# Kernel tuning notes

Hardware: AMD Instinct MI355X
Metric: run time of the kernel (lower is better)

The kernel has to match this reference:

```python
import jax, jax.numpy as jnp
import numpy as np

B, T, NI, NH, NO = 32, 2048, 1, 512, 1


def setup_inputs() -> dict:
    key = jax.random.key(0)
    ks = jax.random.split(key, 7)
    x = jax.random.normal(ks[0], (B, T, NI), dtype=jnp.float32)
    # torch code draws h_0 ~ U[-1,1) once and tiles over batch; here per-batch uniform
    h_0 = jax.random.uniform(ks[1], (B, NH), dtype=jnp.float32) * 2.0 - 1.0
    w_input_std = 1.0 / np.sqrt(NH)
    W_ih = jax.random.normal(ks[2], (NH, NI), dtype=jnp.float32) * w_input_std
    prob_c = 0.1
    w_hidden_std = 1.5 / np.sqrt(prob_c * NH)
    mask = jax.random.bernoulli(ks[3], prob_c, (NH, NH)).astype(jnp.float32)
    W_hh = jax.random.normal(ks[4], (NH, NH), dtype=jnp.float32) * w_hidden_std * mask
    W_hz = jax.random.normal(ks[5], (NO, NH), dtype=jnp.float32) * w_input_std
    W_zh = jax.random.uniform(ks[6], (NH, NO), dtype=jnp.float32, minval=-1.0, maxval=1.0)
    return {"x": x, "h_0": h_0, "W_ih": W_ih, "W_hh": W_hh, "W_hz": W_hz, "W_zh": W_zh}


def reference(x, h_0, W_ih, W_hh, W_hz, W_zh):
    dt, tau = 0.001, 0.01
    alpha = dt / tau  # 0.1
    # precompute input projection for all timesteps: [T, B, NH]
    x_proj = jnp.einsum('bti,hi->tbh', x, W_ih)

    def step(carry, xp_t):
        h_prev, z_prev = carry  # [B,NH], [B,NO]
        h_transfer = jnp.tanh(h_prev)
        dhdt = -h_prev + h_transfer @ W_hh.T + xp_t + z_prev @ W_zh.T
        h_t = h_prev + alpha * dhdt
        z_t = jnp.tanh(h_t) @ W_hz.T
        return (h_t, z_t), (h_t, z_t)

    z0 = jnp.tanh(h_0) @ W_hz.T
    _, (h, z) = jax.lax.scan(step, (h_0, z0), x_proj)
    # scan stacks time first -> [T,B,*]; transpose to [B,T,*]
    return jnp.swapaxes(z, 0, 1), jnp.swapaxes(h, 0, 1)
```

## Files before the change

### kernel.cpp

```cpp
#include <hip/hip_runtime.h>


#define NH   512
#define TT   2048
#define BB   32
#define PAD  96
#define PIN  80

__global__ __launch_bounds__(512) void count_nnz(
    const float* __restrict__ Whh, int* __restrict__ nnz) {
  const int wib  = threadIdx.x >> 6;
  const int lane = threadIdx.x & 63;
  const int row  = blockIdx.x * 8 + wib;
  const float* wrow = Whh + (size_t)row * NH;
  int cnt = 0;
  for (int c = 0; c < NH / 64; ++c)
    cnt += __popcll(__ballot(wrow[c * 64 + lane] != 0.0f));
  if (lane == 0) nnz[row] = cnt;
}

__global__ __launch_bounds__(512) void sort_rows(
    const int* __restrict__ nnz, int* __restrict__ perm) {
  __shared__ int nl[NH];
  const int j = threadIdx.x;
  const int my = nnz[j];
  nl[j] = my;
  __syncthreads();
  int r = 0;
  const int4* p4 = (const int4*)nl;
  for (int i = 0; i < NH / 4; ++i) {
    int4 v = p4[i];
    const int base = i * 4;
    r += (v.x > my) || (v.x == my && base + 0 < j);
    r += (v.y > my) || (v.y == my && base + 1 < j);
    r += (v.z > my) || (v.z == my && base + 2 < j);
    r += (v.w > my) || (v.w == my && base + 3 < j);
  }
  perm[r] = j;
}

__global__ __launch_bounds__(64) void build_schedule(
    const float* __restrict__ Whh, const int* __restrict__ perm,
    float* __restrict__ vals, unsigned* __restrict__ offs,
    int* __restrict__ cntw) {
  __shared__ int claim[2][32];
  const int lane = threadIdx.x;
  const int wid  = blockIdx.x;
  const int p    = wid * 64 + lane;
  const int half = lane >> 5;
  const int home = lane & 31;
  const int row  = perm[p];
  const float* wrow = Whh + (size_t)row * NH;

  unsigned occ32[16];
  int remaining = 0;
  unsigned nonempty = 0;
  #pragma unroll
  for (int r = 0; r < 16; ++r) {
    unsigned lo = 0, hi = 0;
    #pragma unroll
    for (int m = 0; m < 16; ++m) {
      lo |= (wrow[(2 * r)     + 32 * m] != 0.f) ? (1u << m) : 0u;
      hi |= (wrow[(2 * r + 1) + 32 * m] != 0.f) ? (1u << m) : 0u;
    }
    occ32[r] = lo | (hi << 16);
    remaining += __popc(lo) + __popc(hi);
    if (lo) nonempty |= 1u << (2 * r);
    if (hi) nonempty |= 1u << (2 * r + 1);
  }

  int s = 0;
  while (__ballot(remaining > 0) != 0ull && s < PAD) {
    claim[half][home] = 0;
    __builtin_amdgcn_wave_barrier();

    bool placed = false;
    int  mybank = 0;
    unsigned excl = 0;
    const int key = (remaining << 8) | (lane + 1);

    for (int round = 0; round < 12; ++round) {
      unsigned cand = (placed || remaining == 0) ? 0u : (nonempty & ~excl);
      bool want = cand != 0u;
      int bl = 0;
      if (want) {
        unsigned rot = home ? ((cand >> home) | (cand << (32 - home))) : cand;
        bl = (home + __ffs(rot) - 1) & 31;
      }
      if (__ballot(want) == 0ull) break;
      if (want) atomicMax(&claim[half][bl], key);
      __builtin_amdgcn_wave_barrier();
      if (want) {
        int c = ((volatile int*)claim[half])[bl];
        if (c == key) {
          placed = true; mybank = bl;
          ((volatile int*)claim[half])[bl] = 0x7FFFFFFF;
        } else {
          excl |= 1u << bl;
        }
      }
      __builtin_amdgcn_wave_barrier();
    }

    if (!placed && remaining > 0 && (PAD - s) <= remaining) {
      placed = true;
      mybank = __ffs(nonempty) - 1;
    }

    float v = 0.f; unsigned col = 0u;
    if (placed) {
      #pragma unroll
      for (int r = 0; r < 16; ++r) {
        if (r == (mybank >> 1)) {
          unsigned w   = occ32[r];
          unsigned m16 = (mybank & 1) ? (w >> 16) : (w & 0xFFFFu);
          int m = __ffs(m16) - 1;
          col = (unsigned)(mybank + 32 * m);
          unsigned nm = m16 & (m16 - 1u);
          occ32[r] = (mybank & 1) ? ((w & 0x0000FFFFu) | (nm << 16))
                                  : ((w & 0xFFFF0000u) | nm);
          if (nm == 0u) nonempty &= ~(1u << mybank);
        }
      }
      v = wrow[col];
      --remaining;
    }
    vals[s * NH + p] = v;
    offs[s * NH + p] = col;
    ++s;
  }
  if (lane == 0) cntw[wid] = s;
  for (int e = s; e < PAD; ++e) {
    vals[e * NH + p] = 0.f;
    offs[e * NH + p] = 0u;
  }
}

template <int CTRL, int RM>
__device__ __forceinline__ float dppadd(float v) {
  int t = __builtin_amdgcn_update_dpp(0, __float_as_int(v), CTRL, RM, 0xF, true);
  return v + __int_as_float(t);
}
__device__ __forceinline__ float wave_sum_lane63(float v) {
  v = dppadd<0xB1,  0xF>(v);
  v = dppadd<0x4E,  0xF>(v);
  v = dppadd<0x141, 0xF>(v);
  v = dppadd<0x140, 0xF>(v);
  v = dppadd<0x142, 0xA>(v);
  v = dppadd<0x143, 0xC>(v);
  return v;
}

__device__ __forceinline__ float ftanh(float x) {
  float xc = fminf(9.0f, fmaxf(-9.0f, x));
  float t  = __expf(2.0f * xc);
  return (t - 1.0f) * __builtin_amdgcn_rcpf(t + 1.0f);
}

#define GA(T_RD, E) (*(const float*)((const char*)(T_RD) + cidx[E]))

#define ESN_STEP(T_RD, T_WR, RWR, SIDX)                                      \
  {                                                                          \
    float d0 = 0.f, d1 = 0.f, d2 = 0.f, d3 = 0.f;                            \
    _Pragma("unroll")                                                        \
    for (int e = 0; e < PAD; e += 8) {                                       \
      if (e < cw) {                                                          \
        d0 = fmaf(wval[e + 0], GA(T_RD, e + 0), d0);                         \
        d1 = fmaf(wval[e + 1], GA(T_RD, e + 1), d1);                         \
        d2 = fmaf(wval[e + 2], GA(T_RD, e + 2), d2);                         \
        d3 = fmaf(wval[e + 3], GA(T_RD, e + 3), d3);                         \
        d0 = fmaf(wval[e + 4], GA(T_RD, e + 4), d0);                         \
        d1 = fmaf(wval[e + 5], GA(T_RD, e + 5), d1);                         \
        d2 = fmaf(wval[e + 6], GA(T_RD, e + 6), d2);                         \
        d3 = fmaf(wval[e + 7], GA(T_RD, e + 7), d3);                         \
      }                                                                      \
    }                                                                        \
    float dot  = (d0 + d1) + (d2 + d3);                                      \
    float xp   = x_lds[SIDX] * w_ih;                                         \
    float dhdt = ((dot - h) + xp) + z_prev * w_zh;                           \
    float hn   = h + 0.1f * dhdt;                                            \
    float thn  = ftanh(hn);                                                  \
    T_WR[row] = thn;                                                         \
    oh[(SIDX) * NH + row] = hn;                                              \
    float pzs = wave_sum_lane63(thn * w_hz);                                 \
    if (lane == 63) red[RWR][wid] = pzs;                                     \
    asm volatile("s_waitcnt lgkmcnt(0)\n\ts_barrier" ::: "memory");          \
    float4 r0 = *(const float4*)&red[RWR][0];                                \
    float4 r1 = *(const float4*)&red[RWR][4];                                \
    float z = ((r0.x + r0.y) + (r0.z + r0.w)) + ((r1.x + r1.y) + (r1.z + r1.w)); \
    if (p == 0) oz[SIDX] = z;                                                \
    z_prev = z; h = hn;                                                      \
  }

__global__ __launch_bounds__(512, 2) void esn_steps(
    const float* __restrict__ x,   const float* __restrict__ h0,
    const float* __restrict__ Wih, const float* __restrict__ Whz,
    const float* __restrict__ Wzh, const float* __restrict__ vals,
    const unsigned* __restrict__ offs, const int* __restrict__ perm,
    const int* __restrict__ cntw, float* __restrict__ out) {
  __shared__ float t_lds[2][NH];
  __shared__ float x_lds[TT];
  __shared__ __align__(16) float red[2][8];

  const int p    = threadIdx.x;
  const int b    = blockIdx.x;
  const int lane = p & 63;
  const int wid  = p >> 6;
  const int row  = perm[p];

  float* t0 = t_lds[0];
  float* t1 = t_lds[1];

  for (int i = p; i < TT; i += NH) x_lds[i] = x[(size_t)b * TT + i];

  int cw = __builtin_amdgcn_readfirstlane((cntw[wid] + 7) & ~7);

  float    wval[PAD];
  unsigned cidx[PAD];
  #pragma unroll
  for (int e = 0; e < PAD; ++e) {
    wval[e] = vals[e * NH + p];
    cidx[e] = offs[e * NH + p] * 4u;
  }
  #pragma unroll
  for (int e = 0; e < PIN; ++e)
    asm volatile("" : "+v"(wval[e]), "+v"(cidx[e]));

  const float w_ih = Wih[row];
  const float w_hz = Whz[row];
  const float w_zh = Wzh[row];
  float h = h0[(size_t)b * NH + row];

  float* oz = out + (size_t)b * TT;
  float* oh = out + (size_t)BB * TT + (size_t)b * TT * NH;

  float th0 = ftanh(h);
  t0[row] = th0;
  float pz = wave_sum_lane63(th0 * w_hz);
  if (lane == 63) red[0][wid] = pz;
  __syncthreads();
  float4 i0 = *(const float4*)&red[0][0];
  float4 i1 = *(const float4*)&red[0][4];
  float z_prev = ((i0.x + i0.y) + (i0.z + i0.w)) + ((i1.x + i1.y) + (i1.z + i1.w));

  for (int s = 0; s < TT; s += 2) {
    ESN_STEP(t0, t1, 1, s);
    ESN_STEP(t1, t0, 0, s + 1);
  }
}

extern "C" void kernel_launch(void* const* d_in, const int* in_sizes, int n_in,
                              void* d_out, int out_size, void* d_ws,
                              size_t ws_size, hipStream_t stream) {
  const float* x   = (const float*)d_in[0];
  const float* h0  = (const float*)d_in[1];
  const float* Wih = (const float*)d_in[2];
  const float* Whh = (const float*)d_in[3];
  const float* Whz = (const float*)d_in[4];
  const float* Wzh = (const float*)d_in[5];
  float* out = (float*)d_out;

  float*    vals = (float*)d_ws;
  unsigned* offs = (unsigned*)(vals + PAD * NH);
  int*      nnz  = (int*)(offs + PAD * NH);
  int*      perm = nnz + NH;
  int*      cntw = perm + NH;

  hipLaunchKernelGGL(count_nnz, dim3(NH / 8), dim3(512), 0, stream, Whh, nnz);
  hipLaunchKernelGGL(sort_rows, dim3(1), dim3(512), 0, stream, nnz, perm);
  hipLaunchKernelGGL(build_schedule, dim3(8), dim3(64), 0, stream,
                     Whh, perm, vals, offs, cntw);
  hipLaunchKernelGGL(esn_steps, dim3(BB), dim3(512), 0, stream,
                     x, h0, Wih, Whz, Wzh, vals, offs, perm, cntw, out);
}
```

Before: 2.640 ms.

## Replace greedy bank-claim scheduler with bipartite edge coloring for sparse W_hh

The per-slot greedy bank-claiming scheduler is replaced by a bipartite edge-coloring routine that uses alternating-path recoloring (in the style of König's theorem) to assign each nonzero of a row to a slot. No two lanes in a half-wave then read the same LDS bank in the same slot. The goal is to shrink the number of padded slots (cntw) and remove bank conflicts in the recurrent sparse matvec that runs for every timestep. The cost is a serial single-thread coloring in the setup kernel, which adds preprocessing latency on every call.

Result: slower. 3.196 ms (+21.0%).

```diff
diff --git a/kernel.cpp b/kernel.cpp
--- a/kernel.cpp
+++ b/kernel.cpp
@@ -6,6 +6,7 @@
 #define BB   32
 #define PAD  96
 #define PIN  80
+#define NONE_ 0xFF
 
 __global__ __launch_bounds__(512) void count_nnz(
     const float* __restrict__ Whh, int* __restrict__ nnz) {
@@ -39,100 +40,158 @@
   perm[r] = j;
 }
 
-__global__ __launch_bounds__(64) void build_schedule(
+__global__ __launch_bounds__(64) void build_color(
     const float* __restrict__ Whh, const int* __restrict__ perm,
     float* __restrict__ vals, unsigned* __restrict__ offs,
     int* __restrict__ cntw) {
-  __shared__ int claim[2][32];
+  __shared__ unsigned short occ[64][32];
+  __shared__ unsigned char  mL[2][32][PAD];
+  __shared__ unsigned char  mB[2][32][PAD];
+  __shared__ unsigned freeL[2][32][3];
+  __shared__ unsigned freeB[2][32][3];
+  __shared__ short pB[2][128], pL[2][128];
+  __shared__ int cwsh;
+
   const int lane = threadIdx.x;
-  const int wid  = blockIdx.x;
-  const int p    = wid * 64 + lane;
-  const int half = lane >> 5;
-  const int home = lane & 31;
+  const int g    = blockIdx.x;
+  const int p    = g * 64 + lane;
+  const int hl   = lane >> 5;
+  const int li   = lane & 31;
   const int row  = perm[p];
   const float* wrow = Whh + (size_t)row * NH;
 
-  unsigned occ32[16];
-  int remaining = 0;
-  unsigned nonempty = 0;
+  if (lane == 0) cwsh = 0;
+  for (int b = 0; b < 32; ++b) {
+    unsigned m16 = 0;
+    for (int m = 0; m < 16; ++m)
+      m16 |= (wrow[b + 32 * m] != 0.f) ? (1u << m) : 0u;
+    occ[lane][b] = (unsigned short)m16;
+  }
+  for (int c = 0; c < PAD; ++c) { mL[hl][li][c] = NONE_; mB[hl][li][c] = NONE_; }
   #pragma unroll
-  for (int r = 0; r < 16; ++r) {
-    unsigned lo = 0, hi = 0;
-    #pragma unroll
-    for (int m = 0; m < 16; ++m) {
-      lo |= (wrow[(2 * r)     + 32 * m] != 0.f) ? (1u << m) : 0u;
-      hi |= (wrow[(2 * r + 1) + 32 * m] != 0.f) ? (1u << m) : 0u;
-    }
-    occ32[r] = lo | (hi << 16);
-    remaining += __popc(lo) + __popc(hi);
-    if (lo) nonempty |= 1u << (2 * r);
-    if (hi) nonempty |= 1u << (2 * r + 1);
-  }
-
-  int s = 0;
-  while (__ballot(remaining > 0) != 0ull && s < PAD) {
-    claim[half][home] = 0;
-    __builtin_amdgcn_wave_barrier();
-
-    bool placed = false;
-    int  mybank = 0;
-    unsigned excl = 0;
-    const int key = (remaining << 8) | (lane + 1);
-
-    for (int round = 0; round < 12; ++round) {
-      unsigned cand = (placed || remaining == 0) ? 0u : (nonempty & ~excl);
-      bool want = cand != 0u;
-      int bl = 0;
-      if (want) {
-        unsigned rot = home ? ((cand >> home) | (cand << (32 - home))) : cand;
-        bl = (home + __ffs(rot) - 1) & 31;
-      }
-      if (__ballot(want) == 0ull) break;
-      if (want) atomicMax(&claim[half][bl], key);
-      __builtin_amdgcn_wave_barrier();
-      if (want) {
-        int c = ((volatile int*)claim[half])[bl];
-        if (c == key) {
-          placed = true; mybank = bl;
-          ((volatile int*)claim[half])[bl] = 0x7FFFFFFF;
-        } else {
-          excl |= 1u << bl;
+  for (int w2 = 0; w2 < 3; ++w2) {
+    freeL[hl][li][w2] = 0xFFFFFFFFu;
+    freeB[hl][li][w2] = 0xFFFFFFFFu;
+  }
+  __syncthreads();
+
+  if (li == 0) {
+    int maxc = 0;
+    for (int l = 0; l < 32; ++l) {
+      const int gl = hl * 32 + l;
+      for (int b = 0; b < 32; ++b) {
+        const int mult = __popc((unsigned)occ[gl][b]);
+        for (int m = 0; m < mult; ++m) {
+          int c = -1;
+          #pragma unroll
+          for (int w2 = 0; w2 < 3; ++w2) {
+            unsigned cm = freeL[hl][l][w2] & freeB[hl][b][w2];
+            if (cm) { c = w2 * 32 + __ffs(cm) - 1; break; }
+          }
+          if (c >= 0) {
+            mL[hl][l][c] = (unsigned char)b;
+            mB[hl][b][c] = (unsigned char)l;
+            freeL[hl][l][c >> 5] &= ~(1u << (c & 31));
+            freeB[hl][b][c >> 5] &= ~(1u << (c & 31));
+            if (c > maxc) maxc = c;
+            continue;
+          }
+          int a = -1, be = -1;
+          #pragma unroll
+          for (int w2 = 0; w2 < 3; ++w2) {
+            unsigned mm = freeL[hl][l][w2];
+            if (mm) { a = w2 * 32 + __ffs(mm) - 1; break; }
+          }
+          #pragma unroll
+          for (int w2 = 0; w2 < 3; ++w2) {
+            unsigned mm = freeB[hl][b][w2];
+            if (mm) { be = w2 * 32 + __ffs(mm) - 1; break; }
+          }
+          if (a < 0) continue;
+          if (be < 0) {
+            mL[hl][l][a] = (unsigned char)b;
+            freeL[hl][l][a >> 5] &= ~(1u << (a & 31));
+            if (a > maxc) maxc = a;
+            continue;
+          }
+          int n = 0, curN = b, curCol = a, isbank = 1, of = 0;
+          for (;;) {
+            int nxt = isbank ? (int)mB[hl][curN][curCol]
+                             : (int)mL[hl][curN][curCol];
+            if (nxt == NONE_) break;
+            if (n >= 128) { of = 1; break; }
+            pB[hl][n] = (short)(isbank ? curN : nxt);
+            pL[hl][n] = (short)(isbank ? nxt : curN);
+            ++n;
+            curN = nxt; isbank ^= 1;
+            curCol = (curCol == a) ? be : a;
+          }
+          if (of) {
+            mL[hl][l][a] = (unsigned char)b;
+            freeL[hl][l][a >> 5] &= ~(1u << (a & 31));
+            if (a > maxc) maxc = a;
+            continue;
+          }
+          for (int i = 0; i < n; ++i) {
+            int oc = (i & 1) ? be : a;
+            mB[hl][pB[hl][i]][oc] = NONE_;
+            mL[hl][pL[hl][i]][oc] = NONE_;
+          }
+          for (int i = 0; i < n; ++i) {
+            int nc = (i & 1) ? a : be;
+            mB[hl][pB[hl][i]][nc] = (unsigned char)pL[hl][i];
+            mL[hl][pL[hl][i]][nc] = (unsigned char)pB[hl][i];
+          }
+          freeB[hl][b][a >> 5]  ^= (1u << (a & 31));
+          freeB[hl][b][be >> 5] ^= (1u << (be & 31));
+          if (isbank) {
+            freeB[hl][curN][a >> 5]  ^= (1u << (a & 31));
+            freeB[hl][curN][be >> 5] ^= (1u << (be & 31));
+          } else {
+            freeL[hl][curN][a >> 5]  ^= (1u << (a & 31));
+            freeL[hl][curN][be >> 5] ^= (1u << (be & 31));
+          }
+          mL[hl][l][a] = (unsigned char)b;
+          mB[hl][b][a] = (unsigned char)l;
+          freeL[hl][l][a >> 5] &= ~(1u << (a & 31));
+          freeB[hl][b][a >> 5] &= ~(1u << (a & 31));
+          if (a > maxc) maxc = a;
         }
       }
-      __builtin_amdgcn_wave_barrier();
     }
-
-    if (!placed && remaining > 0 && (PAD - s) <= remaining) {
-      placed = true;
-      mybank = __ffs(nonempty) - 1;
+    atomicMax(&cwsh, maxc + 1);
+  }
+  __syncthreads();
+
+  for (int b = 0; b < 32; ++b) {
+    int need = __popc((unsigned)occ[lane][b]);
+    int have = 0;
+    for (int c = 0; c < PAD; ++c) have += (mL[hl][li][c] == b);
+    while (have < need) {
+      for (int c = 0; c < PAD; ++c)
+        if (mL[hl][li][c] == NONE_) {
+          mL[hl][li][c] = (unsigned char)b;
+          atomicMax(&cwsh, c + 1);
+          break;
+        }
+      ++have;
     }
-
+  }
+  __syncthreads();
+  if (lane == 0) cntw[g] = cwsh;
+
+  for (int c = 0; c < PAD; ++c) {
+    int b = mL[hl][li][c];
     float v = 0.f; unsigned col = 0u;
-    if (placed) {
-      #pragma unroll
-      for (int r = 0; r < 16; ++r) {
-        if (r == (mybank >> 1)) {
-          unsigned w   = occ32[r];
-          unsigned m16 = (mybank & 1) ? (w >> 16) : (w & 0xFFFFu);
-          int m = __ffs(m16) - 1;
-          col = (unsigned)(mybank + 32 * m);
-          unsigned nm = m16 & (m16 - 1u);
-          occ32[r] = (mybank & 1) ? ((w & 0x0000FFFFu) | (nm << 16))
-                                  : ((w & 0xFFFF0000u) | nm);
-          if (nm == 0u) nonempty &= ~(1u << mybank);
-        }
-      }
+    if (b != NONE_) {
+      unsigned m16 = (unsigned)occ[lane][b];
+      int m = __ffs(m16) - 1;
+      occ[lane][b] = (unsigned short)(m16 & (m16 - 1u));
+      col = (unsigned)(b + 32 * m);
       v = wrow[col];
-      --remaining;
     }
-    vals[s * NH + p] = v;
-    offs[s * NH + p] = col;
-    ++s;
-  }
-  if (lane == 0) cntw[wid] = s;
-  for (int e = s; e < PAD; ++e) {
-    vals[e * NH + p] = 0.f;
-    offs[e * NH + p] = 0u;
+    vals[c * NH + p] = v;
+    offs[c * NH + p] = col;
   }
 }
 
@@ -268,7 +327,7 @@
 
   hipLaunchKernelGGL(count_nnz, dim3(NH / 8), dim3(512), 0, stream, Whh, nnz);
   hipLaunchKernelGGL(sort_rows, dim3(1), dim3(512), 0, stream, nnz, perm);
-  hipLaunchKernelGGL(build_schedule, dim3(8), dim3(64), 0, stream,
+  hipLaunchKernelGGL(build_color, dim3(8), dim3(64), 0, stream,
                      Whh, perm, vals, offs, cntw);
   hipLaunchKernelGGL(esn_steps, dim3(BB), dim3(512), 0, stream,
                      x, h0, Wih, Whz, Wzh, vals, offs, perm, cntw, out);
```

## Balance bank load across wave halves and prefer dense banks in sparse schedule

Applied to the files above, without the earlier changes.

The sparse W_hh schedule builder now runs as one 512-thread block. Within each wave it greedily reorders rows so that the two 32-lane halves carry balanced per-bank loads, which produces a second permutation used by the step kernel. The per-slot bank claim now prefers banks that still hold many nonzeros (at least 4, then at least 2) and runs fewer claim rounds. The goal is fewer padded slots per wave (a lower cntw) and fewer LDS bank conflicts in the recurrent gather, at the cost of a slower single-block preprocessing kernel.

Measured after the change: 2.679 ms. Within noise of the previous version (+1.5%).

```diff
diff --git a/kernel.cpp b/kernel.cpp
--- a/kernel.cpp
+++ b/kernel.cpp
@@ -39,98 +39,148 @@
   perm[r] = j;
 }
 
-__global__ __launch_bounds__(64) void build_schedule(
+__global__ __launch_bounds__(512) void build_psched(
     const float* __restrict__ Whh, const int* __restrict__ perm,
-    float* __restrict__ vals, unsigned* __restrict__ offs,
-    int* __restrict__ cntw) {
-  __shared__ int claim[2][32];
-  const int lane = threadIdx.x;
-  const int wid  = blockIdx.x;
-  const int p    = wid * 64 + lane;
-  const int half = lane >> 5;
-  const int home = lane & 31;
-  const int row  = perm[p];
+    int* __restrict__ perm2, float* __restrict__ vals,
+    unsigned* __restrict__ offs, int* __restrict__ cntw) {
+  __shared__ unsigned short occ[8][64][32];
+  __shared__ unsigned char  lorder[8][64];
+  __shared__ int   claim[8][2][32];
+  __shared__ short bload[8][2][32];
+  __shared__ short cnth[8][2];
+
+  const int tid  = threadIdx.x;
+  const int w    = tid >> 6;
+  const int lane = tid & 63;
+  const int hl   = (lane >> 5) & 1;
+  const int li   = lane & 31;
+
+  for (int r = 0; r < 64; ++r) {
+    const int rw = perm[w * 64 + r];
+    const float* wr = Whh + (size_t)rw * NH;
+    unsigned m16 = 0;
+    for (int c = 0; c < 8; ++c) {
+      unsigned long long bal = __ballot(wr[c * 64 + lane] != 0.0f);
+      if (lane < 32) {
+        m16 |= ((unsigned)((bal >> lane) & 1ull)) << (2 * c);
+        m16 |= ((unsigned)((bal >> (lane + 32)) & 1ull)) << (2 * c + 1);
+      }
+    }
+    if (lane < 32) occ[w][r][lane] = (unsigned short)m16;
+  }
+  if (lane < 32) { bload[w][0][lane] = 0; bload[w][1][lane] = 0; }
+  if (lane == 0) { cnth[w][0] = 0; cnth[w][1] = 0; }
+  __builtin_amdgcn_wave_barrier();
+
+  for (int r = 0; r < 64; ++r) {
+    int cb = 0, t0 = 0, t1 = 0;
+    if (lane < 32) {
+      cb = __popc((unsigned)occ[w][r][lane]);
+      t0 = bload[w][0][lane] + cb;
+      t1 = bload[w][1][lane] + cb;
+    }
+    int m0 = t0, m1 = t1;
+    #pragma unroll
+    for (int o = 32; o > 0; o >>= 1) {
+      int u0 = __shfl_xor(m0, o), u1 = __shfl_xor(m1, o);
+      m0 = u0 > m0 ? u0 : m0;
+      m1 = u1 > m1 ? u1 : m1;
+    }
+    int c0 = cnth[w][0], c1 = cnth[w][1];
+    int h;
+    if (c0 >= 32) h = 1;
+    else if (c1 >= 32) h = 0;
+    else h = (m1 < m0) ? 1 : 0;
+    if (lane < 32) bload[w][h][lane] = (short)(bload[w][h][lane] + cb);
+    if (lane == 0) {
+      lorder[w][h * 32 + (h ? c1 : c0)] = (unsigned char)r;
+      cnth[w][h] = (short)((h ? c1 : c0) + 1);
+    }
+    __builtin_amdgcn_wave_barrier();
+  }
+
+  const int o   = lorder[w][lane];
+  const int row = perm[w * 64 + o];
+  const int p   = w * 64 + lane;
+  perm2[p] = row;
+  unsigned short* myocc = occ[w][o];
   const float* wrow = Whh + (size_t)row * NH;
-
-  unsigned occ32[16];
-  int remaining = 0;
-  unsigned nonempty = 0;
-  #pragma unroll
-  for (int r = 0; r < 16; ++r) {
-    unsigned lo = 0, hi = 0;
+  unsigned bmAll = 0, bm2 = 0, bm4 = 0;
+  int rem = 0;
+  for (int b = 0; b < 32; ++b) {
+    int m = __popc((unsigned)myocc[b]);
+    rem += m;
+    if (m >= 1) bmAll |= 1u << b;
+    if (m >= 2) bm2   |= 1u << b;
+    if (m >= 4) bm4   |= 1u << b;
+  }
+
+  int c = 0;
+  while (__ballot(rem > 0) != 0ull && c < PAD) {
+    claim[w][hl][li] = 0;
+    __builtin_amdgcn_wave_barrier();
+    const int  key   = (rem << 6) | (li + 1);
+    const bool force = (PAD - c) <= rem;
+    bool placed = false; int myb = 0;
+    unsigned excl = 0;
+
     #pragma unroll
-    for (int m = 0; m < 16; ++m) {
-      lo |= (wrow[(2 * r)     + 32 * m] != 0.f) ? (1u << m) : 0u;
-      hi |= (wrow[(2 * r + 1) + 32 * m] != 0.f) ? (1u << m) : 0u;
-    }
-    occ32[r] = lo | (hi << 16);
-    remaining += __popc(lo) + __popc(hi);
-    if (lo) nonempty |= 1u << (2 * r);
-    if (hi) nonempty |= 1u << (2 * r + 1);
-  }
-
-  int s = 0;
-  while (__ballot(remaining > 0) != 0ull && s < PAD) {
-    claim[half][home] = 0;
-    __builtin_amdgcn_wave_barrier();
-
-    bool placed = false;
-    int  mybank = 0;
-    unsigned excl = 0;
-    const int key = (remaining << 8) | (lane + 1);
-
-    for (int round = 0; round < 12; ++round) {
-      unsigned cand = (placed || remaining == 0) ? 0u : (nonempty & ~excl);
-      bool want = cand != 0u;
-      int bl = 0;
+    for (int round = 0; round < 4; ++round) {
+      bool want = !placed && rem > 0;
+      int b = 0;
       if (want) {
-        unsigned rot = home ? ((cand >> home) | (cand << (32 - home))) : cand;
-        bl = (home + __ffs(rot) - 1) & 31;
+        unsigned cand = bmAll & ~excl;
+        unsigned pref = cand & bm4;
+        if (!pref) pref = cand & bm2;
+        if (!pref) pref = cand;
+        if (!pref) { want = false; }
+        else {
+          unsigned rot = li ? ((pref >> li) | (pref << (32 - li))) : pref;
+          b = (li + __ffs(rot) - 1) & 31;
+        }
       }
       if (__ballot(want) == 0ull) break;
-      if (want) atomicMax(&claim[half][bl], key);
-      __builtin_amdgcn_wave_barrier();
+      bool win = false;
       if (want) {
-        int c = ((volatile int*)claim[half])[bl];
-        if (c == key) {
-          placed = true; mybank = bl;
-          ((volatile int*)claim[half])[bl] = 0x7FFFFFFF;
+        if (force) {
+          win = true;
         } else {
-          excl |= 1u << bl;
+          atomicMax(&claim[w][hl][b], key);
+          __builtin_amdgcn_wave_barrier();
+          int cv = ((volatile int*)claim[w][hl])[b];
+          if (cv == key) {
+            win = true;
+            ((volatile int*)claim[w][hl])[b] = 0x7FFFFFFF;
+          } else {
+            excl |= 1u << b;
+          }
         }
       }
       __builtin_amdgcn_wave_barrier();
-    }
-
-    if (!placed && remaining > 0 && (PAD - s) <= remaining) {
-      placed = true;
-      mybank = __ffs(nonempty) - 1;
+      if (win) { placed = true; myb = b; }
     }
 
     float v = 0.f; unsigned col = 0u;
     if (placed) {
-      #pragma unroll
-      for (int r = 0; r < 16; ++r) {
-        if (r == (mybank >> 1)) {
-          unsigned w   = occ32[r];
-          unsigned m16 = (mybank & 1) ? (w >> 16) : (w & 0xFFFFu);
-          int m = __ffs(m16) - 1;
-          col = (unsigned)(mybank + 32 * m);
-          unsigned nm = m16 & (m16 - 1u);
-          occ32[r] = (mybank & 1) ? ((w & 0x0000FFFFu) | (nm << 16))
-                                  : ((w & 0xFFFF0000u) | nm);
-          if (nm == 0u) nonempty &= ~(1u << mybank);
-        }
-      }
+      unsigned m16 = (unsigned)myocc[myb];
+      int m = __ffs(m16) - 1;
+      col = (unsigned)(myb + 32 * m);
+      unsigned nm16 = m16 & (m16 - 1u);
+      myocc[myb] = (unsigned short)nm16;
+      int nm = __popc(nm16);
+      unsigned bit = 1u << myb;
+      bmAll = (nm >= 1) ? (bmAll | bit) : (bmAll & ~bit);
+      bm2   = (nm >= 2) ? (bm2   | bit) : (bm2   & ~bit);
+      bm4   = (nm >= 4) ? (bm4   | bit) : (bm4   & ~bit);
       v = wrow[col];
-      --remaining;
-    }
-    vals[s * NH + p] = v;
-    offs[s * NH + p] = col;
-    ++s;
-  }
-  if (lane == 0) cntw[wid] = s;
-  for (int e = s; e < PAD; ++e) {
+      --rem;
+    }
+    vals[c * NH + p] = v;
+    offs[c * NH + p] = col;
+    ++c;
+  }
+  if (lane == 0) cntw[w] = c;
+  for (int e = c; e < PAD; ++e) {
     vals[e * NH + p] = 0.f;
     offs[e * NH + p] = 0u;
   }
@@ -196,7 +246,7 @@
     const float* __restrict__ x,   const float* __restrict__ h0,
     const float* __restrict__ Wih, const float* __restrict__ Whz,
     const float* __restrict__ Wzh, const float* __restrict__ vals,
-    const unsigned* __restrict__ offs, const int* __restrict__ perm,
+    const unsigned* __restrict__ offs, const int* __restrict__ perm2,
     const int* __restrict__ cntw, float* __restrict__ out) {
   __shared__ float t_lds[2][NH];
   __shared__ float x_lds[TT];
@@ -206,7 +256,7 @@
   const int b    = blockIdx.x;
   const int lane = p & 63;
   const int wid  = p >> 6;
-  const int row  = perm[p];
+  const int row  = perm2[p];
 
   float* t0 = t_lds[0];
   float* t1 = t_lds[1];
@@ -260,16 +310,17 @@
   const float* Wzh = (const float*)d_in[5];
   float* out = (float*)d_out;
 
-  float*    vals = (float*)d_ws;
-  unsigned* offs = (unsigned*)(vals + PAD * NH);
-  int*      nnz  = (int*)(offs + PAD * NH);
-  int*      perm = nnz + NH;
-  int*      cntw = perm + NH;
+  float*    vals  = (float*)d_ws;
+  unsigned* offs  = (unsigned*)(vals + PAD * NH);
+  int*      nnz   = (int*)(offs + PAD * NH);
+  int*      perm  = nnz + NH;
+  int*      perm2 = perm + NH;
+  int*      cntw  = perm2 + NH;
 
   hipLaunchKernelGGL(count_nnz, dim3(NH / 8), dim3(512), 0, stream, Whh, nnz);
   hipLaunchKernelGGL(sort_rows, dim3(1), dim3(512), 0, stream, nnz, perm);
-  hipLaunchKernelGGL(build_schedule, dim3(8), dim3(64), 0, stream,
-                     Whh, perm, vals, offs, cntw);
+  hipLaunchKernelGGL(build_psched, dim3(1), dim3(512), 0, stream,
+                     Whh, perm, perm2, vals, offs, cntw);
   hipLaunchKernelGGL(esn_steps, dim3(BB), dim3(512), 0, stream,
-                     x, h0, Wih, Whz, Wzh, vals, offs, perm, cntw, out);
-}
+                     x, h0, Wih, Whz, Wzh, vals, offs, perm2, cntw, out);
+}
```
